# Kernel optimization log

Measured on AMD Instinct MI355X. Metric: run time of the kernel, lower is better.

The kernel has to match this reference:

```python
import jax, jax.numpy as jnp
import numpy as np

A = 512   # input channels
B = 32    # number of capsule types
H4 = 16   # h*h pose dims per capsule


def setup_inputs() -> dict:
    key = jax.random.key(0)
    k1, k2, k3, k4, k5 = jax.random.split(key, 5)
    # Input feature map [N, A, H, W]
    x = jax.random.normal(k1, (64, A, 32, 32), dtype=jnp.float32)
    # Fused weights: B parallel 1x1 convs concatenated along out-channel dim.
    # Pose convs: B x Conv2d(A -> 16, k=1) -> [B*16, A]; activation convs: B x Conv2d(A -> 1) -> [B, A]
    bound = 1.0 / np.sqrt(A)  # PyTorch Conv2d default init range
    W_pose = jax.random.uniform(k2, (B * H4, A), minval=-bound, maxval=bound, dtype=jnp.float32)
    b_pose = jax.random.uniform(k3, (B * H4,), minval=-bound, maxval=bound, dtype=jnp.float32)
    W_act = jax.random.uniform(k4, (B, A), minval=-bound, maxval=bound, dtype=jnp.float32)
    b_act = jax.random.uniform(k5, (B,), minval=-bound, maxval=bound, dtype=jnp.float32)
    return {"x": x, "W_pose": W_pose, "b_pose": b_pose, "W_act": W_act, "b_act": b_act}


def reference(x, W_pose, b_pose, W_act, b_act):
    # 1x1 conv == channel contraction; fuse all 2*B tiny convs into two GEMMs.
    # poses: [N, B*16, H, W]
    poses = jnp.einsum('nahw,oa->nohw', x, W_pose) + b_pose[None, :, None, None]
    # activations: sigmoid([N, B, H, W])
    activations = jax.nn.sigmoid(jnp.einsum('nahw,oa->nohw', x, W_act) + b_act[None, :, None, None])
    return poses, activations
```

## Files before the change

### kernel.cpp

```cpp
#include <hip/hip_runtime.h>
#include <hip/hip_bf16.h>


typedef __attribute__((ext_vector_type(8))) short short8;
typedef __attribute__((ext_vector_type(4))) float f32x4;

#define A_CH   512
#define HW     1024
#define N_B    64
#define O_POSE 512
#define O_ACT  32
#define O_TOT  544
#define TO     128
#define TM     256
#define BK     32
#define NIT    (A_CH / BK)

__device__ __forceinline__ unsigned pk(float lo, float hi) {
    __hip_bfloat162 h = __float22bfloat162_rn(make_float2(lo, hi));
    return *reinterpret_cast<unsigned*>(&h);
}

__global__ __launch_bounds__(512, 4) void caps_fused_gemm(
    const float* __restrict__ x,
    const float* __restrict__ Wp,
    const float* __restrict__ bp,
    const float* __restrict__ Wa,
    const float* __restrict__ ba,
    float* __restrict__ out)
{
    __shared__ __align__(16) short ldsA[2][TO * BK];
    __shared__ __align__(16) short ldsB[2][TM * BK];

    const int tid = threadIdx.x;
    const int n   = blockIdx.z;
    const int o0  = blockIdx.y * TO;
    const int m0  = blockIdx.x * TM;

    const float* xn = x + (size_t)n * A_CH * HW + m0;

    const int ao = tid >> 2;
    const int ak = (tid & 3) * 8;
    const float* arow = nullptr;
    {
        int R = o0 + ao;
        if (R < O_POSE)     arow = Wp + (size_t)R * A_CH + ak;
        else if (R < O_TOT) arow = Wa + (size_t)(R - O_POSE) * A_CH + ak;
    }
    const int bm = tid & 255;
    const int bk = (tid >> 8) * 16;
    const float* bbase = xn + (size_t)bk * HW + bm;

    float4 a0, a1;
    float  breg[16];

    auto load_tiles = [&](int k0) {
        if (arow) {
            a0 = *(const float4*)(arow + k0);
            a1 = *(const float4*)(arow + k0 + 4);
        } else {
            a0 = make_float4(0.f, 0.f, 0.f, 0.f);
            a1 = a0;
        }
#pragma unroll
        for (int j = 0; j < 16; ++j)
            breg[j] = bbase[(size_t)(k0 + j) * HW];
    };

    const int aswz = 8 * ((ao >> 1) & 3);
    const int bswz = 8 * ((bm >> 1) & 3);

    auto store_tiles = [&](int buf) {
        short8 av;
        ((unsigned*)&av)[0] = pk(a0.x, a0.y);
        ((unsigned*)&av)[1] = pk(a0.z, a0.w);
        ((unsigned*)&av)[2] = pk(a1.x, a1.y);
        ((unsigned*)&av)[3] = pk(a1.z, a1.w);
        *(short8*)&ldsA[buf][ao * BK + (ak ^ aswz)] = av;

        short8 b0, b1;
#pragma unroll
        for (int j = 0; j < 4; ++j) {
            ((unsigned*)&b0)[j] = pk(breg[2 * j], breg[2 * j + 1]);
            ((unsigned*)&b1)[j] = pk(breg[8 + 2 * j], breg[9 + 2 * j]);
        }
        *(short8*)&ldsB[buf][bm * BK + (bk ^ bswz)]       = b0;
        *(short8*)&ldsB[buf][bm * BK + ((bk + 8) ^ bswz)] = b1;
    };

    const int lane = tid & 63;
    const int w    = tid >> 6;
    const int wo   = (w >> 2) * 64;
    const int wm   = (w & 3) * 64;
    const int l16  = lane & 15;
    const int g    = lane >> 4;

    f32x4 acc[4][4] = {};

    load_tiles(0);
    store_tiles(0);
    __syncthreads();

    for (int it = 0; it < NIT; ++it) {
        const int cur = it & 1;
        short8 aF[4], bF[4];
#pragma unroll
        for (int f = 0; f < 4; ++f) {
            int r = wo + f * 16 + l16;
            aF[f] = *(const short8*)&ldsA[cur][r * BK + ((g * 8) ^ (8 * ((r >> 1) & 3)))];
            int c = wm + f * 16 + l16;
            bF[f] = *(const short8*)&ldsB[cur][c * BK + ((g * 8) ^ (8 * ((c >> 1) & 3)))];
        }
        if (it + 1 < NIT) load_tiles((it + 1) * BK);
#pragma unroll
        for (int fo = 0; fo < 4; ++fo)
#pragma unroll
            for (int fm = 0; fm < 4; ++fm)
                acc[fo][fm] = __builtin_amdgcn_mfma_f32_16x16x32_bf16(
                    aF[fo], bF[fm], acc[fo][fm], 0, 0, 0);
        if (it + 1 < NIT) store_tiles(cur ^ 1);
        __syncthreads();
    }

    float* actOut = out + (size_t)N_B * O_POSE * HW;
    const size_t poseN = (size_t)n * O_POSE * HW;
    const size_t actN  = (size_t)n * O_ACT * HW;
#pragma unroll
    for (int fo = 0; fo < 4; ++fo) {
#pragma unroll
        for (int i = 0; i < 4; ++i) {
            int R = o0 + wo + fo * 16 + g * 4 + i;
            if (R >= O_TOT) continue;
            if (R < O_POSE) {
                float bias = bp[R];
#pragma unroll
                for (int fm = 0; fm < 4; ++fm) {
                    int cc = m0 + wm + fm * 16 + l16;
                    __builtin_nontemporal_store(acc[fo][fm][i] + bias,
                                                &out[poseN + (size_t)R * HW + cc]);
                }
            } else {
                float bias = ba[R - O_POSE];
#pragma unroll
                for (int fm = 0; fm < 4; ++fm) {
                    int cc = m0 + wm + fm * 16 + l16;
                    float v = acc[fo][fm][i] + bias;
                    __builtin_nontemporal_store(1.0f / (1.0f + __expf(-v)),
                                                &actOut[actN + (size_t)(R - O_POSE) * HW + cc]);
                }
            }
        }
    }
}

extern "C" void kernel_launch(void* const* d_in, const int* in_sizes, int n_in,
                              void* d_out, int out_size, void* d_ws, size_t ws_size,
                              hipStream_t stream) {
    (void)in_sizes; (void)n_in; (void)d_ws; (void)ws_size; (void)out_size;
    const float* x  = (const float*)d_in[0];
    const float* Wp = (const float*)d_in[1];
    const float* bp = (const float*)d_in[2];
    const float* Wa = (const float*)d_in[3];
    const float* ba = (const float*)d_in[4];
    dim3 grid(HW / TM, (O_TOT + TO - 1) / TO, N_B);
    caps_fused_gemm<<<grid, dim3(512), 0, stream>>>(x, Wp, bp, Wa, ba, (float*)d_out);
}
```

Measured before the change: 290.3 us.

## Pre-convert weights to bf16 and cover all output channels per block

```diff
diff --git a/kernel.cpp b/kernel.cpp
--- a/kernel.cpp
+++ b/kernel.cpp
@@ -11,140 +11,134 @@
 #define O_POSE 512
 #define O_ACT  32
 #define O_TOT  544
-#define TO     128
-#define TM     256
-#define BK     32
+#define O_PAD  576
+#define TM     64
+#define BK     64
 #define NIT    (A_CH / BK)
+#define NOF    9
 
 __device__ __forceinline__ unsigned pk(float lo, float hi) {
     __hip_bfloat162 h = __float22bfloat162_rn(make_float2(lo, hi));
     return *reinterpret_cast<unsigned*>(&h);
 }
 
-__global__ __launch_bounds__(512, 4) void caps_fused_gemm(
+__global__ __launch_bounds__(256) void prep_w(const float* __restrict__ Wp,
+                                              const float* __restrict__ Wa,
+                                              unsigned short* __restrict__ Wb) {
+    const int r = blockIdx.x;
+    const int c = threadIdx.x * 2;
+    float2 v = make_float2(0.f, 0.f);
+    if (r < O_POSE)     v = *(const float2*)(Wp + (size_t)r * A_CH + c);
+    else if (r < O_TOT) v = *(const float2*)(Wa + (size_t)(r - O_POSE) * A_CH + c);
+    __hip_bfloat162 h = __float22bfloat162_rn(v);
+    *(unsigned*)(Wb + (size_t)r * A_CH + c) = *reinterpret_cast<unsigned*>(&h);
+}
+
+__global__ __launch_bounds__(256, 2) void caps_gemm(
     const float* __restrict__ x,
-    const float* __restrict__ Wp,
+    const unsigned short* __restrict__ Wb,
     const float* __restrict__ bp,
-    const float* __restrict__ Wa,
     const float* __restrict__ ba,
     float* __restrict__ out)
 {
-    __shared__ __align__(16) short ldsA[2][TO * BK];
-    __shared__ __align__(16) short ldsB[2][TM * BK];
+    __shared__ __align__(16) short lds[2][TM * BK];
 
     const int tid = threadIdx.x;
-    const int n   = blockIdx.z;
-    const int o0  = blockIdx.y * TO;
     const int m0  = blockIdx.x * TM;
+    const int n   = blockIdx.y;
 
     const float* xn = x + (size_t)n * A_CH * HW + m0;
 
-    const int ao = tid >> 2;
-    const int ak = (tid & 3) * 8;
-    const float* arow = nullptr;
-    {
-        int R = o0 + ao;
-        if (R < O_POSE)     arow = Wp + (size_t)R * A_CH + ak;
-        else if (R < O_TOT) arow = Wa + (size_t)(R - O_POSE) * A_CH + ak;
-    }
-    const int bm = tid & 255;
-    const int bk = (tid >> 8) * 16;
-    const float* bbase = xn + (size_t)bk * HW + bm;
+    const int sm = tid & 63;
+    const int sk = (tid >> 6) * 16;
+    const float* sbase = xn + (size_t)sk * HW + sm;
 
-    float4 a0, a1;
-    float  breg[16];
+    const int s0   = sk >> 3;
+    const int wswz = sm & 7;
+    const int wr0  = sm * BK + ((s0 ^ wswz) << 3);
+    const int wr1  = sm * BK + (((s0 + 1) ^ wswz) << 3);
 
-    auto load_tiles = [&](int k0) {
-        if (arow) {
-            a0 = *(const float4*)(arow + k0);
-            a1 = *(const float4*)(arow + k0 + 4);
-        } else {
-            a0 = make_float4(0.f, 0.f, 0.f, 0.f);
-            a1 = a0;
-        }
+    float xr[16];
+    auto load_x = [&](int it) {
 #pragma unroll
         for (int j = 0; j < 16; ++j)
-            breg[j] = bbase[(size_t)(k0 + j) * HW];
+            xr[j] = sbase[(size_t)(it * BK + j) * HW];
     };
-
-    const int aswz = 8 * ((ao >> 1) & 3);
-    const int bswz = 8 * ((bm >> 1) & 3);
-
-    auto store_tiles = [&](int buf) {
-        short8 av;
-        ((unsigned*)&av)[0] = pk(a0.x, a0.y);
-        ((unsigned*)&av)[1] = pk(a0.z, a0.w);
-        ((unsigned*)&av)[2] = pk(a1.x, a1.y);
-        ((unsigned*)&av)[3] = pk(a1.z, a1.w);
-        *(short8*)&ldsA[buf][ao * BK + (ak ^ aswz)] = av;
-
-        short8 b0, b1;
+    auto store_x = [&](int buf) {
+        short8 v0, v1;
 #pragma unroll
         for (int j = 0; j < 4; ++j) {
-            ((unsigned*)&b0)[j] = pk(breg[2 * j], breg[2 * j + 1]);
-            ((unsigned*)&b1)[j] = pk(breg[8 + 2 * j], breg[9 + 2 * j]);
+            ((unsigned*)&v0)[j] = pk(xr[2 * j],     xr[2 * j + 1]);
+            ((unsigned*)&v1)[j] = pk(xr[8 + 2 * j], xr[9 + 2 * j]);
         }
-        *(short8*)&ldsB[buf][bm * BK + (bk ^ bswz)]       = b0;
-        *(short8*)&ldsB[buf][bm * BK + ((bk + 8) ^ bswz)] = b1;
+        *(short8*)&lds[buf][wr0] = v0;
+        *(short8*)&lds[buf][wr1] = v1;
     };
 
     const int lane = tid & 63;
     const int w    = tid >> 6;
-    const int wo   = (w >> 2) * 64;
-    const int wm   = (w & 3) * 64;
     const int l16  = lane & 15;
     const int g    = lane >> 4;
 
-    f32x4 acc[4][4] = {};
+    const unsigned short* wlane = Wb + (size_t)(w * 144 + l16) * A_CH + g * 8;
 
-    load_tiles(0);
-    store_tiles(0);
+    int bidx[4];
+#pragma unroll
+    for (int fm = 0; fm < 4; ++fm) bidx[fm] = (fm * 16 + l16) * BK;
+    const int bswz = l16 & 7;
+
+    f32x4 acc[NOF][4] = {};
+
+    load_x(0);
+    store_x(0);
     __syncthreads();
 
     for (int it = 0; it < NIT; ++it) {
         const int cur = it & 1;
-        short8 aF[4], bF[4];
+        if (it + 1 < NIT) load_x(it + 1);
 #pragma unroll
-        for (int f = 0; f < 4; ++f) {
-            int r = wo + f * 16 + l16;
-            aF[f] = *(const short8*)&ldsA[cur][r * BK + ((g * 8) ^ (8 * ((r >> 1) & 3)))];
-            int c = wm + f * 16 + l16;
-            bF[f] = *(const short8*)&ldsB[cur][c * BK + ((g * 8) ^ (8 * ((c >> 1) & 3)))];
-        }
-        if (it + 1 < NIT) load_tiles((it + 1) * BK);
-#pragma unroll
-        for (int fo = 0; fo < 4; ++fo)
+        for (int ks = 0; ks < 2; ++ks) {
+            short8 bF[4];
 #pragma unroll
             for (int fm = 0; fm < 4; ++fm)
-                acc[fo][fm] = __builtin_amdgcn_mfma_f32_16x16x32_bf16(
-                    aF[fo], bF[fm], acc[fo][fm], 0, 0, 0);
-        if (it + 1 < NIT) store_tiles(cur ^ 1);
+                bF[fm] = *(const short8*)&lds[cur][bidx[fm] + (((ks * 4 + g) ^ bswz) << 3)];
+#pragma unroll
+            for (int of = 0; of < NOF; ++of) {
+                short8 aF = *(const short8*)(wlane + (size_t)of * 16 * A_CH + it * BK + ks * 32);
+#pragma unroll
+                for (int fm = 0; fm < 4; ++fm)
+                    acc[of][fm] = __builtin_amdgcn_mfma_f32_16x16x32_bf16(
+                        aF, bF[fm], acc[of][fm], 0, 0, 0);
+            }
+        }
+        if (it + 1 < NIT) store_x(cur ^ 1);
         __syncthreads();
     }
 
     float* actOut = out + (size_t)N_B * O_POSE * HW;
     const size_t poseN = (size_t)n * O_POSE * HW;
     const size_t actN  = (size_t)n * O_ACT * HW;
+    const int ob = w * 144;
 #pragma unroll
-    for (int fo = 0; fo < 4; ++fo) {
+    for (int of = 0; of < NOF; ++of) {
 #pragma unroll
         for (int i = 0; i < 4; ++i) {
-            int R = o0 + wo + fo * 16 + g * 4 + i;
+            const int R = ob + of * 16 + g * 4 + i;
             if (R >= O_TOT) continue;
             if (R < O_POSE) {
-                float bias = bp[R];
+                const float bias = bp[R];
 #pragma unroll
                 for (int fm = 0; fm < 4; ++fm) {
-                    int cc = m0 + wm + fm * 16 + l16;
-                    __builtin_nontemporal_store(acc[fo][fm][i] + bias,
+                    const int cc = m0 + fm * 16 + l16;
+                    __builtin_nontemporal_store(acc[of][fm][i] + bias,
                                                 &out[poseN + (size_t)R * HW + cc]);
                 }
             } else {
-                float bias = ba[R - O_POSE];
+                const float bias = ba[R - O_POSE];
 #pragma unroll
                 for (int fm = 0; fm < 4; ++fm) {
-                    int cc = m0 + wm + fm * 16 + l16;
-                    float v = acc[fo][fm][i] + bias;
+                    const int cc = m0 + fm * 16 + l16;
+                    const float v = acc[of][fm][i] + bias;
                     __builtin_nontemporal_store(1.0f / (1.0f + __expf(-v)),
                                                 &actOut[actN + (size_t)(R - O_POSE) * HW + cc]);
                 }
@@ -156,12 +150,14 @@
 extern "C" void kernel_launch(void* const* d_in, const int* in_sizes, int n_in,
                               void* d_out, int out_size, void* d_ws, size_t ws_size,
                               hipStream_t stream) {
-    (void)in_sizes; (void)n_in; (void)d_ws; (void)ws_size; (void)out_size;
+    (void)in_sizes; (void)n_in; (void)out_size; (void)ws_size;
     const float* x  = (const float*)d_in[0];
     const float* Wp = (const float*)d_in[1];
     const float* bp = (const float*)d_in[2];
     const float* Wa = (const float*)d_in[3];
     const float* ba = (const float*)d_in[4];
-    dim3 grid(HW / TM, (O_TOT + TO - 1) / TO, N_B);
-    caps_fused_gemm<<<grid, dim3(512), 0, stream>>>(x, Wp, bp, Wa, ba, (float*)d_out);
+    unsigned short* Wb = (unsigned short*)d_ws;
+
+    prep_w<<<dim3(O_PAD), dim3(256), 0, stream>>>(Wp, Wa, Wb);
+    caps_gemm<<<dim3(HW / TM, N_B), dim3(256), 0, stream>>>(x, Wb, bp, ba, (float*)d_out);
 }
```

New measurement: 296.7 us. 1.02x slower.
